# Kernel optimization log

Measured on AMD Instinct MI355X. Metric: run time of the kernel, lower is better.

The kernel has to match this reference:

```python
import jax, jax.numpy as jnp
import numpy as np

EPS = 0.1
B, D, H = 1048576, 2, 64


def _lagrangian(xs, W0, b0, W1, b1, W2, b2, W3, b3):
    # xs: [2] single sample -> scalar Lagrangian L(q, v)
    h = jnp.tanh(xs @ W0 + b0)
    h = jnp.tanh(h @ W1 + b1)
    h = jnp.tanh(h @ W2 + b2)
    return (h @ W3 + b3)[0]


def setup_inputs() -> dict:
    key = jax.random.key(0)
    ks = jax.random.split(key, 9)
    def lin(k, fan_in, fan_out):
        # mimic nn.Linear default init U(-1/sqrt(fan_in), 1/sqrt(fan_in))
        bound = 1.0 / np.sqrt(fan_in)
        kw, kb = jax.random.split(k)
        W = jax.random.uniform(kw, (fan_in, fan_out), jnp.float32, -bound, bound)
        b = jax.random.uniform(kb, (fan_out,), jnp.float32, -bound, bound)
        return W, b
    W0, b0 = lin(ks[1], D, H)
    W1, b1 = lin(ks[2], H, H)
    W2, b2 = lin(ks[3], H, H)
    W3, b3 = lin(ks[4], H, 1)
    x = jax.random.normal(ks[0], (B, D), jnp.float32)
    return {"t": 0, "x": x, "W0": W0, "b0": b0, "W1": W1, "b1": b1,
            "W2": W2, "b2": b2, "W3": W3, "b3": b3}


def reference(t, x, W0, b0, W1, b1, W2, b2, W3, b3):
    lag = lambda xs: _lagrangian(xs, W0, b0, W1, b1, W2, b2, W3, b3)
    grad_all = jax.vmap(jax.grad(lag))(x)          # [B, 2]
    H_full = jax.vmap(jax.hessian(lag))(x)          # [B, 2, 2]
    dL_dq = grad_all[:, 0:1]                        # [B, 1]
    d2L_dqv = H_full[:, 1, 0:1]                     # d2L/(dv dq)
    d2L_dv2 = H_full[:, 1, 1:2]                     # d2L/dv2
    v = x[:, 1:2]
    a = (dL_dq - d2L_dqv * v) / (d2L_dv2 + EPS)
    return jnp.concatenate([v, a], axis=1)          # [B, 2]
```

## Files before the change

### kernel.cpp

```cpp
#include <hip/hip_runtime.h>
#include <hip/hip_fp16.h>

typedef _Float16 half8 __attribute__((ext_vector_type(8)));
typedef float    f32x4 __attribute__((ext_vector_type(4)));
typedef float    f32x2 __attribute__((ext_vector_type(2)));

#define EPSL 0.1f
#define TWO_LOG2E 2.8853900817779268f
#define NT 4

#if __has_builtin(__builtin_amdgcn_exp2f)
#define EXP2(x) __builtin_amdgcn_exp2f(x)
#else
#define EXP2(x) __expf((x) * 0.6931471805599453f)
#endif

__device__ __forceinline__ f32x2 tanh2s(f32x2 y) {
    f32x2 e;
    e.x = EXP2(y.x);
    e.y = EXP2(y.y);
    const f32x2 ep = e + 1.0f;
    f32x2 r;
    r.x = __builtin_amdgcn_rcpf(ep.x);
    r.y = __builtin_amdgcn_rcpf(ep.y);
    return 1.0f - 2.0f * r;
}

__device__ __forceinline__ unsigned int pk2(float a, float b) {
    union { __fp16 __attribute__((ext_vector_type(2))) h; unsigned int u; } v;
    v.h = __builtin_amdgcn_cvt_pkrtz(a, b);
    return v.u;
}
__device__ __forceinline__ f32x2 unpk2v(unsigned int u) {
    union { unsigned int u; __half2 h; } v; v.u = u;
    const float2 f = __half22float2(v.h);
    return (f32x2){f.x, f.y};
}
__device__ __forceinline__ f32x2 lo2(f32x4 v) { return __builtin_shufflevector(v, v, 0, 1); }
__device__ __forceinline__ f32x2 hi2(f32x4 v) { return __builtin_shufflevector(v, v, 2, 3); }

union frag_u { unsigned int u[4]; half8 h; };

__global__ void pack_weights(const float* __restrict__ W1,
                             const float* __restrict__ W2,
                             _Float16* __restrict__ pk) {
    const int t = threadIdx.x;
    const int combo = blockIdx.x;
    const int mt  = combo & 3;
    const int kt  = (combo >> 2) & 1;
    const int mat = combo >> 3;
    const int q = t >> 4, r = t & 15;
    _Float16 v[8];
    #pragma unroll
    for (int j = 0; j < 8; ++j) {
        const int fk = (2 * kt + (j >> 2)) * 16 + 4 * q + (j & 3);
        float x;
        if (mat == 0)      x = W1[(kt * 32 + 8 * q + j) * 64 + mt * 16 + r];
        else if (mat == 1) x = W2[fk * 64 + mt * 16 + r];
        else if (mat == 2) x = W2[(mt * 16 + r) * 64 + fk];
        else {
            const int f0 = (mt & 1) * 32 + 8 * (r >> 2) + ((mt >> 1) & 1) * 4 + (r & 3);
            x = W1[f0 * 64 + fk];
        }
        v[j] = (_Float16)x;
    }
    *(half8*)(pk + combo * 512 + t * 8) = *(const half8*)v;
}

extern "C" __global__ void __launch_bounds__(256)
lnn_mfma(const float* __restrict__ x,
         const float* __restrict__ W0, const float* __restrict__ b0,
         const float* __restrict__ b1, const float* __restrict__ b2,
         const float* __restrict__ W3,
         const _Float16* __restrict__ pk,
         float* __restrict__ out)
{
    __shared__ float occ_pad[19456];
    if (blockIdx.x == 0xFFFFFFFFu) ((volatile float*)occ_pad)[threadIdx.x] = 1.0f;

    const int t = threadIdx.x & 63;
    const int q = t >> 4;
    const int r = t & 15;
    const long sbase = (long)blockIdx.x * (64 * NT) + (threadIdx.x >> 6) * (16 * NT);

    float x0v[NT], x1v[NT];
    #pragma unroll
    for (int u = 0; u < NT; ++u) {
        const float2 xv = *(const float2*)(x + 2 * (sbase + u * 16 + r));
        x0v[u] = xv.x; x1v[u] = xv.y;
    }

    auto ldpk = [&](int mat, int kt, int mt) -> half8 {
        return *(const half8*)(pk + ((mat * 2 + kt) * 4 + mt) * 512 + t * 8);
    };

    half8 ah0[NT][2], at0[NT][2];
    #pragma unroll
    for (int kt = 0; kt < 2; ++kt) {
        const int f = kt * 32 + q * 8;
        const float4 waA = *(const float4*)(W0 + f);
        const float4 waB = *(const float4*)(W0 + f + 4);
        const float4 wbA = *(const float4*)(W0 + 64 + f);
        const float4 wbB = *(const float4*)(W0 + 64 + f + 4);
        const float4 bbA = *(const float4*)(b0 + f);
        const float4 bbB = *(const float4*)(b0 + f + 4);
        const f32x2 wa2[4] = {{waA.x,waA.y},{waA.z,waA.w},{waB.x,waB.y},{waB.z,waB.w}};
        const f32x2 wb2[4] = {{wbA.x,wbA.y},{wbA.z,wbA.w},{wbB.x,wbB.y},{wbB.z,wbB.w}};
        const f32x2 bb2[4] = {{bbA.x,bbA.y},{bbA.z,bbA.w},{bbB.x,bbB.y},{bbB.z,bbB.w}};
        #pragma unroll
        for (int u = 0; u < NT; ++u) {
            union { unsigned int uu[4]; half8 h; } ph, pt;
            #pragma unroll
            for (int p = 0; p < 4; ++p) {
                const f32x2 z = x0v[u] * wa2[p] + x1v[u] * wb2[p] + bb2[p];
                const f32x2 h = tanh2s(z * TWO_LOG2E);
                const f32x2 A = 1.0f - h * h;
                const f32x2 tt = A * wb2[p];
                ph.uu[p] = pk2(h.x, h.y);
                pt.uu[p] = pk2(tt.x, tt.y);
            }
            ah0[u][kt] = ph.h; at0[u][kt] = pt.h;
        }
    }

    f32x4 acc[NT][4], tacc[NT][4];
    #pragma unroll
    for (int mt = 0; mt < 4; ++mt) {
        const f32x4 bv = *(const f32x4*)(b1 + mt * 16 + 4 * q);
        #pragma unroll
        for (int u = 0; u < NT; ++u) {
            acc[u][mt] = bv;
            tacc[u][mt] = (f32x4){0,0,0,0};
        }
    }
    #pragma unroll
    for (int kt = 0; kt < 2; ++kt)
        #pragma unroll
        for (int mt = 0; mt < 4; ++mt) {
            const half8 aw = ldpk(0, kt, mt);
            #pragma unroll
            for (int u = 0; u < NT; ++u) {
                acc[u][mt]  = __builtin_amdgcn_mfma_f32_16x16x32_f16(aw, ah0[u][kt], acc[u][mt], 0, 0, 0);
                tacc[u][mt] = __builtin_amdgcn_mfma_f32_16x16x32_f16(aw, at0[u][kt], tacc[u][mt], 0, 0, 0);
            }
        }

    frag_u bh1[NT][2], bt1[NT][2];
    #pragma unroll
    for (int u = 0; u < NT; ++u)
        #pragma unroll
        for (int mt = 0; mt < 4; ++mt) {
            const f32x2 zp[2] = {lo2(acc[u][mt]),  hi2(acc[u][mt])};
            const f32x2 tp[2] = {lo2(tacc[u][mt]), hi2(tacc[u][mt])};
            #pragma unroll
            for (int p = 0; p < 2; ++p) {
                const f32x2 h  = tanh2s(zp[p] * TWO_LOG2E);
                const f32x2 A  = 1.0f - h * h;
                const f32x2 th = A * tp[p];
                bh1[u][mt >> 1].u[2 * (mt & 1) + p] = pk2(h.x, h.y);
                bt1[u][mt >> 1].u[2 * (mt & 1) + p] = pk2(th.x, th.y);
            }
        }

    #pragma unroll
    for (int mt = 0; mt < 4; ++mt) {
        const f32x4 bv = *(const f32x4*)(b2 + mt * 16 + 4 * q);
        #pragma unroll
        for (int u = 0; u < NT; ++u) {
            acc[u][mt] = bv;
            tacc[u][mt] = (f32x4){0,0,0,0};
        }
    }
    #pragma unroll
    for (int kt = 0; kt < 2; ++kt)
        #pragma unroll
        for (int mt = 0; mt < 4; ++mt) {
            const half8 aw = ldpk(1, kt, mt);
            #pragma unroll
            for (int u = 0; u < NT; ++u) {
                acc[u][mt]  = __builtin_amdgcn_mfma_f32_16x16x32_f16(aw, bh1[u][kt].h, acc[u][mt], 0, 0, 0);
                tacc[u][mt] = __builtin_amdgcn_mfma_f32_16x16x32_f16(aw, bt1[u][kt].h, tacc[u][mt], 0, 0, 0);
            }
        }

    frag_u bh2[NT][2], bt2[NT][2];
    #pragma unroll
    for (int mt = 0; mt < 4; ++mt) {
        const float4 w3v = *(const float4*)(W3 + mt * 16 + 4 * q);
        const f32x2 w3p[2] = {{w3v.x, w3v.y}, {w3v.z, w3v.w}};
        #pragma unroll
        for (int u = 0; u < NT; ++u) {
            const f32x2 zp[2] = {lo2(acc[u][mt]),  hi2(acc[u][mt])};
            const f32x2 tp[2] = {lo2(tacc[u][mt]), hi2(tacc[u][mt])};
            #pragma unroll
            for (int p = 0; p < 2; ++p) {
                const f32x2 h  = tanh2s(zp[p] * TWO_LOG2E);
                const f32x2 A  = 1.0f - h * h;
                const f32x2 dz = A * w3p[p];
                const f32x2 t1 = h * tp[p];
                const f32x2 td = -2.0f * (dz * t1);
                bh2[u][mt >> 1].u[2 * (mt & 1) + p] = pk2(dz.x, dz.y);
                bt2[u][mt >> 1].u[2 * (mt & 1) + p] = pk2(td.x, td.y);
            }
        }
    }

    #pragma unroll
    for (int u = 0; u < NT; ++u)
        #pragma unroll
        for (int mt = 0; mt < 4; ++mt) { acc[u][mt] = (f32x4){0,0,0,0}; tacc[u][mt] = (f32x4){0,0,0,0}; }
    #pragma unroll
    for (int kt = 0; kt < 2; ++kt)
        #pragma unroll
        for (int mt = 0; mt < 4; ++mt) {
            const half8 aw = ldpk(2, kt, mt);
            #pragma unroll
            for (int u = 0; u < NT; ++u) {
                acc[u][mt]  = __builtin_amdgcn_mfma_f32_16x16x32_f16(aw, bh2[u][kt].h, acc[u][mt], 0, 0, 0);
                tacc[u][mt] = __builtin_amdgcn_mfma_f32_16x16x32_f16(aw, bt2[u][kt].h, tacc[u][mt], 0, 0, 0);
            }
        }

    frag_u bd[NT][2], btd[NT][2];
    #pragma unroll
    for (int u = 0; u < NT; ++u)
        #pragma unroll
        for (int mt = 0; mt < 4; ++mt) {
            const f32x2 gp[2] = {lo2(acc[u][mt]),  hi2(acc[u][mt])};
            const f32x2 tp[2] = {lo2(tacc[u][mt]), hi2(tacc[u][mt])};
            #pragma unroll
            for (int p = 0; p < 2; ++p) {
                const f32x2 h  = unpk2v(bh1[u][mt >> 1].u[2 * (mt & 1) + p]);
                const f32x2 th = unpk2v(bt1[u][mt >> 1].u[2 * (mt & 1) + p]);
                const f32x2 A  = 1.0f - h * h;
                const f32x2 d1 = gp[p] * A;
                const f32x2 u2 = (gp[p] * h) * th;
                const f32x2 td = tp[p] * A + (-2.0f) * u2;
                bd[u][mt >> 1].u[2 * (mt & 1) + p]  = pk2(d1.x, d1.y);
                btd[u][mt >> 1].u[2 * (mt & 1) + p] = pk2(td.x, td.y);
            }
        }

    #pragma unroll
    for (int u = 0; u < NT; ++u)
        #pragma unroll
        for (int mt = 0; mt < 4; ++mt) { acc[u][mt] = (f32x4){0,0,0,0}; tacc[u][mt] = (f32x4){0,0,0,0}; }
    #pragma unroll
    for (int kt = 0; kt < 2; ++kt)
        #pragma unroll
        for (int mt = 0; mt < 4; ++mt) {
            const half8 aw = ldpk(3, kt, mt);
            #pragma unroll
            for (int u = 0; u < NT; ++u) {
                acc[u][mt]  = __builtin_amdgcn_mfma_f32_16x16x32_f16(aw, bd[u][kt].h,  acc[u][mt], 0, 0, 0);
                tacc[u][mt] = __builtin_amdgcn_mfma_f32_16x16x32_f16(aw, btd[u][kt].h, tacc[u][mt], 0, 0, 0);
            }
        }

    f32x2 pg2[NT], ph02[NT], ph12[NT];
    #pragma unroll
    for (int u = 0; u < NT; ++u) { pg2[u] = (f32x2){0,0}; ph02[u] = (f32x2){0,0}; ph12[u] = (f32x2){0,0}; }
    #pragma unroll
    for (int mt = 0; mt < 4; ++mt) {
        const int kt = mt & 1;
        const int jb = ((mt >> 1) & 1) * 4;
        const int f  = kt * 32 + q * 8 + jb;
        const float4 waF = *(const float4*)(W0 + f);
        const float4 wbF = *(const float4*)(W0 + 64 + f);
        const f32x2 wa2[2] = {{waF.x, waF.y}, {waF.z, waF.w}};
        const f32x2 wb2[2] = {{wbF.x, wbF.y}, {wbF.z, wbF.w}};
        #pragma unroll
        for (int u = 0; u < NT; ++u) {
            union { half8 h; unsigned int uu[4]; } av; av.h = ah0[u][kt];
            const unsigned int hu[2] = {av.uu[jb >> 1], av.uu[(jb >> 1) + 1]};
            const f32x2 gp[2] = {lo2(acc[u][mt]),  hi2(acc[u][mt])};
            const f32x2 tp[2] = {lo2(tacc[u][mt]), hi2(tacc[u][mt])};
            #pragma unroll
            for (int p = 0; p < 2; ++p) {
                const f32x2 h   = unpk2v(hu[p]);
                const f32x2 A   = 1.0f - h * h;
                const f32x2 th0 = A * wb2[p];
                const f32x2 d0  = gp[p] * A;
                const f32x2 u2  = (gp[p] * h) * th0;
                const f32x2 td0 = tp[p] * A + (-2.0f) * u2;
                pg2[u]  += wa2[p] * d0;
                ph02[u] += wa2[p] * td0;
                ph12[u] += wb2[p] * td0;
            }
        }
    }
    #pragma unroll
    for (int u = 0; u < NT; ++u) {
        float pg  = pg2[u].x  + pg2[u].y;
        float ph0 = ph02[u].x + ph02[u].y;
        float ph1 = ph12[u].x + ph12[u].y;
        pg  += __shfl_xor(pg, 16);  pg  += __shfl_xor(pg, 32);
        ph0 += __shfl_xor(ph0, 16); ph0 += __shfl_xor(ph0, 32);
        ph1 += __shfl_xor(ph1, 16); ph1 += __shfl_xor(ph1, 32);
        if (q == 0) {
            const float num = fmaf(-ph0, x1v[u], pg);
            const float den = ph1 + EPSL;
            const float a = num * __builtin_amdgcn_rcpf(den);
            float2 o;
            o.x = x1v[u];
            o.y = a;
            *(float2*)(out + 2 * (sbase + u * 16 + r)) = o;
        }
    }
}

extern "C" void kernel_launch(void* const* d_in, const int* in_sizes, int n_in,
                              void* d_out, int out_size, void* d_ws, size_t ws_size,
                              hipStream_t stream) {
    const float* x  = (const float*)d_in[1];
    const float* W0 = (const float*)d_in[2];
    const float* b0 = (const float*)d_in[3];
    const float* W1 = (const float*)d_in[4];
    const float* b1 = (const float*)d_in[5];
    const float* W2 = (const float*)d_in[6];
    const float* b2 = (const float*)d_in[7];
    const float* W3 = (const float*)d_in[8];

    _Float16* pk = (_Float16*)d_ws;
    const int B = in_sizes[1] / 2;

    pack_weights<<<32, 64, 0, stream>>>(W1, W2, pk);
    lnn_mfma<<<B / (64 * NT), 256, 0, stream>>>(x, W0, b0, b1, b2, W3, pk, (float*)d_out);
}
```

Before: 215.0 us.

## Switch to persistent grid-stride waves with fewer tiles per wave

Turns the kernel into a persistent one: 768 blocks loop over 16*NT-sample tasks per wave, and the layer-0 weights and biases are hoisted into registers once per thread. NT drops from 4 to 2, which cuts per-wave accumulator register pressure, and the LDS occupancy pad shrinks to match the new occupancy target. The aim is better latency hiding and less launch/tail cost. The risk is less MFMA instruction-level parallelism per wave and a fixed grid size that may not match the CU count.

```diff
diff --git a/kernel.cpp b/kernel.cpp
--- a/kernel.cpp
+++ b/kernel.cpp
@@ -7,7 +7,7 @@
 
 #define EPSL 0.1f
 #define TWO_LOG2E 2.8853900817779268f
-#define NT 4
+#define NT 2
 
 #if __has_builtin(__builtin_amdgcn_exp2f)
 #define EXP2(x) __builtin_amdgcn_exp2f(x)
@@ -73,28 +73,23 @@
          const float* __restrict__ b1, const float* __restrict__ b2,
          const float* __restrict__ W3,
          const _Float16* __restrict__ pk,
-         float* __restrict__ out)
+         float* __restrict__ out,
+         int ntask)
 {
-    __shared__ float occ_pad[19456];
+    __shared__ float occ_pad[13312];
     if (blockIdx.x == 0xFFFFFFFFu) ((volatile float*)occ_pad)[threadIdx.x] = 1.0f;
 
     const int t = threadIdx.x & 63;
     const int q = t >> 4;
     const int r = t & 15;
-    const long sbase = (long)blockIdx.x * (64 * NT) + (threadIdx.x >> 6) * (16 * NT);
-
-    float x0v[NT], x1v[NT];
-    #pragma unroll
-    for (int u = 0; u < NT; ++u) {
-        const float2 xv = *(const float2*)(x + 2 * (sbase + u * 16 + r));
-        x0v[u] = xv.x; x1v[u] = xv.y;
-    }
+    const int wgid = blockIdx.x * 4 + (threadIdx.x >> 6);
+    const int nw   = gridDim.x * 4;
 
     auto ldpk = [&](int mat, int kt, int mt) -> half8 {
         return *(const half8*)(pk + ((mat * 2 + kt) * 4 + mt) * 512 + t * 8);
     };
 
-    half8 ah0[NT][2], at0[NT][2];
+    f32x2 wa2[2][4], wb2[2][4], bb2[2][4];
     #pragma unroll
     for (int kt = 0; kt < 2; ++kt) {
         const int f = kt * 32 + q * 8;
@@ -104,207 +99,220 @@
         const float4 wbB = *(const float4*)(W0 + 64 + f + 4);
         const float4 bbA = *(const float4*)(b0 + f);
         const float4 bbB = *(const float4*)(b0 + f + 4);
-        const f32x2 wa2[4] = {{waA.x,waA.y},{waA.z,waA.w},{waB.x,waB.y},{waB.z,waB.w}};
-        const f32x2 wb2[4] = {{wbA.x,wbA.y},{wbA.z,wbA.w},{wbB.x,wbB.y},{wbB.z,wbB.w}};
-        const f32x2 bb2[4] = {{bbA.x,bbA.y},{bbA.z,bbA.w},{bbB.x,bbB.y},{bbB.z,bbB.w}};
+        wa2[kt][0] = (f32x2){waA.x, waA.y}; wa2[kt][1] = (f32x2){waA.z, waA.w};
+        wa2[kt][2] = (f32x2){waB.x, waB.y}; wa2[kt][3] = (f32x2){waB.z, waB.w};
+        wb2[kt][0] = (f32x2){wbA.x, wbA.y}; wb2[kt][1] = (f32x2){wbA.z, wbA.w};
+        wb2[kt][2] = (f32x2){wbB.x, wbB.y}; wb2[kt][3] = (f32x2){wbB.z, wbB.w};
+        bb2[kt][0] = (f32x2){bbA.x, bbA.y}; bb2[kt][1] = (f32x2){bbA.z, bbA.w};
+        bb2[kt][2] = (f32x2){bbB.x, bbB.y}; bb2[kt][3] = (f32x2){bbB.z, bbB.w};
+    }
+
+    for (int task = wgid; task < ntask; task += nw) {
+        const long sbase = (long)task * (16 * NT);
+
+        float x0v[NT], x1v[NT];
         #pragma unroll
         for (int u = 0; u < NT; ++u) {
-            union { unsigned int uu[4]; half8 h; } ph, pt;
-            #pragma unroll
-            for (int p = 0; p < 4; ++p) {
-                const f32x2 z = x0v[u] * wa2[p] + x1v[u] * wb2[p] + bb2[p];
-                const f32x2 h = tanh2s(z * TWO_LOG2E);
-                const f32x2 A = 1.0f - h * h;
-                const f32x2 tt = A * wb2[p];
-                ph.uu[p] = pk2(h.x, h.y);
-                pt.uu[p] = pk2(tt.x, tt.y);
-            }
-            ah0[u][kt] = ph.h; at0[u][kt] = pt.h;
-        }
-    }
-
-    f32x4 acc[NT][4], tacc[NT][4];
-    #pragma unroll
-    for (int mt = 0; mt < 4; ++mt) {
-        const f32x4 bv = *(const f32x4*)(b1 + mt * 16 + 4 * q);
+            const float2 xv = *(const float2*)(x + 2 * (sbase + u * 16 + r));
+            x0v[u] = xv.x; x1v[u] = xv.y;
+        }
+
+        half8 ah0[NT][2], at0[NT][2];
+        #pragma unroll
+        for (int kt = 0; kt < 2; ++kt)
+            #pragma unroll
+            for (int u = 0; u < NT; ++u) {
+                union { unsigned int uu[4]; half8 h; } ph, pt;
+                #pragma unroll
+                for (int p = 0; p < 4; ++p) {
+                    const f32x2 z = x0v[u] * wa2[kt][p] + x1v[u] * wb2[kt][p] + bb2[kt][p];
+                    const f32x2 h = tanh2s(z * TWO_LOG2E);
+                    const f32x2 A = 1.0f - h * h;
+                    const f32x2 tt = A * wb2[kt][p];
+                    ph.uu[p] = pk2(h.x, h.y);
+                    pt.uu[p] = pk2(tt.x, tt.y);
+                }
+                ah0[u][kt] = ph.h; at0[u][kt] = pt.h;
+            }
+
+        f32x4 acc[NT][4], tacc[NT][4];
+        #pragma unroll
+        for (int mt = 0; mt < 4; ++mt) {
+            const f32x4 bv = *(const f32x4*)(b1 + mt * 16 + 4 * q);
+            #pragma unroll
+            for (int u = 0; u < NT; ++u) {
+                acc[u][mt] = bv;
+                tacc[u][mt] = (f32x4){0,0,0,0};
+            }
+        }
+        #pragma unroll
+        for (int kt = 0; kt < 2; ++kt)
+            #pragma unroll
+            for (int mt = 0; mt < 4; ++mt) {
+                const half8 aw = ldpk(0, kt, mt);
+                #pragma unroll
+                for (int u = 0; u < NT; ++u) {
+                    acc[u][mt]  = __builtin_amdgcn_mfma_f32_16x16x32_f16(aw, ah0[u][kt], acc[u][mt], 0, 0, 0);
+                    tacc[u][mt] = __builtin_amdgcn_mfma_f32_16x16x32_f16(aw, at0[u][kt], tacc[u][mt], 0, 0, 0);
+                }
+            }
+
+        frag_u bh1[NT][2], bt1[NT][2];
+        #pragma unroll
+        for (int u = 0; u < NT; ++u)
+            #pragma unroll
+            for (int mt = 0; mt < 4; ++mt) {
+                const f32x2 zp[2] = {lo2(acc[u][mt]),  hi2(acc[u][mt])};
+                const f32x2 tp[2] = {lo2(tacc[u][mt]), hi2(tacc[u][mt])};
+                #pragma unroll
+                for (int p = 0; p < 2; ++p) {
+                    const f32x2 h  = tanh2s(zp[p] * TWO_LOG2E);
+                    const f32x2 A  = 1.0f - h * h;
+                    const f32x2 th = A * tp[p];
+                    bh1[u][mt >> 1].u[2 * (mt & 1) + p] = pk2(h.x, h.y);
+                    bt1[u][mt >> 1].u[2 * (mt & 1) + p] = pk2(th.x, th.y);
+                }
+            }
+
+        #pragma unroll
+        for (int mt = 0; mt < 4; ++mt) {
+            const f32x4 bv = *(const f32x4*)(b2 + mt * 16 + 4 * q);
+            #pragma unroll
+            for (int u = 0; u < NT; ++u) {
+                acc[u][mt] = bv;
+                tacc[u][mt] = (f32x4){0,0,0,0};
+            }
+        }
+        #pragma unroll
+        for (int kt = 0; kt < 2; ++kt)
+            #pragma unroll
+            for (int mt = 0; mt < 4; ++mt) {
+                const half8 aw = ldpk(1, kt, mt);
+                #pragma unroll
+                for (int u = 0; u < NT; ++u) {
+                    acc[u][mt]  = __builtin_amdgcn_mfma_f32_16x16x32_f16(aw, bh1[u][kt].h, acc[u][mt], 0, 0, 0);
+                    tacc[u][mt] = __builtin_amdgcn_mfma_f32_16x16x32_f16(aw, bt1[u][kt].h, tacc[u][mt], 0, 0, 0);
+                }
+            }
+
+        frag_u bh2[NT][2], bt2[NT][2];
+        #pragma unroll
+        for (int mt = 0; mt < 4; ++mt) {
+            const float4 w3v = *(const float4*)(W3 + mt * 16 + 4 * q);
+            const f32x2 w3p[2] = {{w3v.x, w3v.y}, {w3v.z, w3v.w}};
+            #pragma unroll
+            for (int u = 0; u < NT; ++u) {
+                const f32x2 zp[2] = {lo2(acc[u][mt]),  hi2(acc[u][mt])};
+                const f32x2 tp[2] = {lo2(tacc[u][mt]), hi2(tacc[u][mt])};
+                #pragma unroll
+                for (int p = 0; p < 2; ++p) {
+                    const f32x2 h  = tanh2s(zp[p] * TWO_LOG2E);
+                    const f32x2 A  = 1.0f - h * h;
+                    const f32x2 dz = A * w3p[p];
+                    const f32x2 t1 = h * tp[p];
+                    const f32x2 td = -2.0f * (dz * t1);
+                    bh2[u][mt >> 1].u[2 * (mt & 1) + p] = pk2(dz.x, dz.y);
+                    bt2[u][mt >> 1].u[2 * (mt & 1) + p] = pk2(td.x, td.y);
+                }
+            }
+        }
+
+        #pragma unroll
+        for (int u = 0; u < NT; ++u)
+            #pragma unroll
+            for (int mt = 0; mt < 4; ++mt) { acc[u][mt] = (f32x4){0,0,0,0}; tacc[u][mt] = (f32x4){0,0,0,0}; }
+        #pragma unroll
+        for (int kt = 0; kt < 2; ++kt)
+            #pragma unroll
+            for (int mt = 0; mt < 4; ++mt) {
+                const half8 aw = ldpk(2, kt, mt);
+                #pragma unroll
+                for (int u = 0; u < NT; ++u) {
+                    acc[u][mt]  = __builtin_amdgcn_mfma_f32_16x16x32_f16(aw, bh2[u][kt].h, acc[u][mt], 0, 0, 0);
+                    tacc[u][mt] = __builtin_amdgcn_mfma_f32_16x16x32_f16(aw, bt2[u][kt].h, tacc[u][mt], 0, 0, 0);
+                }
+            }
+
+        frag_u bd[NT][2], btd[NT][2];
+        #pragma unroll
+        for (int u = 0; u < NT; ++u)
+            #pragma unroll
+            for (int mt = 0; mt < 4; ++mt) {
+                const f32x2 gp[2] = {lo2(acc[u][mt]),  hi2(acc[u][mt])};
+                const f32x2 tp[2] = {lo2(tacc[u][mt]), hi2(tacc[u][mt])};
+                #pragma unroll
+                for (int p = 0; p < 2; ++p) {
+                    const f32x2 h  = unpk2v(bh1[u][mt >> 1].u[2 * (mt & 1) + p]);
+                    const f32x2 th = unpk2v(bt1[u][mt >> 1].u[2 * (mt & 1) + p]);
+                    const f32x2 A  = 1.0f - h * h;
+                    const f32x2 d1 = gp[p] * A;
+                    const f32x2 u2 = (gp[p] * h) * th;
+                    const f32x2 td = tp[p] * A + (-2.0f) * u2;
+                    bd[u][mt >> 1].u[2 * (mt & 1) + p]  = pk2(d1.x, d1.y);
+                    btd[u][mt >> 1].u[2 * (mt & 1) + p] = pk2(td.x, td.y);
+                }
+            }
+
+        #pragma unroll
+        for (int u = 0; u < NT; ++u)
+            #pragma unroll
+            for (int mt = 0; mt < 4; ++mt) { acc[u][mt] = (f32x4){0,0,0,0}; tacc[u][mt] = (f32x4){0,0,0,0}; }
+        #pragma unroll
+        for (int kt = 0; kt < 2; ++kt)
+            #pragma unroll
+            for (int mt = 0; mt < 4; ++mt) {
+                const half8 aw = ldpk(3, kt, mt);
+                #pragma unroll
+                for (int u = 0; u < NT; ++u) {
+                    acc[u][mt]  = __builtin_amdgcn_mfma_f32_16x16x32_f16(aw, bd[u][kt].h,  acc[u][mt], 0, 0, 0);
+                    tacc[u][mt] = __builtin_amdgcn_mfma_f32_16x16x32_f16(aw, btd[u][kt].h, tacc[u][mt], 0, 0, 0);
+                }
+            }
+
+        f32x2 pg2[NT], ph02[NT], ph12[NT];
+        #pragma unroll
+        for (int u = 0; u < NT; ++u) { pg2[u] = (f32x2){0,0}; ph02[u] = (f32x2){0,0}; ph12[u] = (f32x2){0,0}; }
+        #pragma unroll
+        for (int mt = 0; mt < 4; ++mt) {
+            const int kt = mt & 1;
+            const int j2 = ((mt >> 1) & 1) * 2;
+            #pragma unroll
+            for (int u = 0; u < NT; ++u) {
+                union { half8 h; unsigned int uu[4]; } av; av.h = ah0[u][kt];
+                const unsigned int hu[2] = {av.uu[j2], av.uu[j2 + 1]};
+                const f32x2 gp[2] = {lo2(acc[u][mt]),  hi2(acc[u][mt])};
+                const f32x2 tp[2] = {lo2(tacc[u][mt]), hi2(tacc[u][mt])};
+                #pragma unroll
+                for (int p = 0; p < 2; ++p) {
+                    const f32x2 h   = unpk2v(hu[p]);
+                    const f32x2 A   = 1.0f - h * h;
+                    const f32x2 th0 = A * wb2[kt][j2 + p];
+                    const f32x2 d0  = gp[p] * A;
+                    const f32x2 u2  = (gp[p] * h) * th0;
+                    const f32x2 td0 = tp[p] * A + (-2.0f) * u2;
+                    pg2[u]  += wa2[kt][j2 + p] * d0;
+                    ph02[u] += wa2[kt][j2 + p] * td0;
+                    ph12[u] += wb2[kt][j2 + p] * td0;
+                }
+            }
+        }
         #pragma unroll
         for (int u = 0; u < NT; ++u) {
-            acc[u][mt] = bv;
-            tacc[u][mt] = (f32x4){0,0,0,0};
-        }
-    }
-    #pragma unroll
-    for (int kt = 0; kt < 2; ++kt)
-        #pragma unroll
-        for (int mt = 0; mt < 4; ++mt) {
-            const half8 aw = ldpk(0, kt, mt);
-            #pragma unroll
-            for (int u = 0; u < NT; ++u) {
-                acc[u][mt]  = __builtin_amdgcn_mfma_f32_16x16x32_f16(aw, ah0[u][kt], acc[u][mt], 0, 0, 0);
-                tacc[u][mt] = __builtin_amdgcn_mfma_f32_16x16x32_f16(aw, at0[u][kt], tacc[u][mt], 0, 0, 0);
-            }
-        }
-
-    frag_u bh1[NT][2], bt1[NT][2];
-    #pragma unroll
-    for (int u = 0; u < NT; ++u)
-        #pragma unroll
-        for (int mt = 0; mt < 4; ++mt) {
-            const f32x2 zp[2] = {lo2(acc[u][mt]),  hi2(acc[u][mt])};
-            const f32x2 tp[2] = {lo2(tacc[u][mt]), hi2(tacc[u][mt])};
-            #pragma unroll
-            for (int p = 0; p < 2; ++p) {
-                const f32x2 h  = tanh2s(zp[p] * TWO_LOG2E);
-                const f32x2 A  = 1.0f - h * h;
-                const f32x2 th = A * tp[p];
-                bh1[u][mt >> 1].u[2 * (mt & 1) + p] = pk2(h.x, h.y);
-                bt1[u][mt >> 1].u[2 * (mt & 1) + p] = pk2(th.x, th.y);
-            }
-        }
-
-    #pragma unroll
-    for (int mt = 0; mt < 4; ++mt) {
-        const f32x4 bv = *(const f32x4*)(b2 + mt * 16 + 4 * q);
-        #pragma unroll
-        for (int u = 0; u < NT; ++u) {
-            acc[u][mt] = bv;
-            tacc[u][mt] = (f32x4){0,0,0,0};
-        }
-    }
-    #pragma unroll
-    for (int kt = 0; kt < 2; ++kt)
-        #pragma unroll
-        for (int mt = 0; mt < 4; ++mt) {
-            const half8 aw = ldpk(1, kt, mt);
-            #pragma unroll
-            for (int u = 0; u < NT; ++u) {
-                acc[u][mt]  = __builtin_amdgcn_mfma_f32_16x16x32_f16(aw, bh1[u][kt].h, acc[u][mt], 0, 0, 0);
-                tacc[u][mt] = __builtin_amdgcn_mfma_f32_16x16x32_f16(aw, bt1[u][kt].h, tacc[u][mt], 0, 0, 0);
-            }
-        }
-
-    frag_u bh2[NT][2], bt2[NT][2];
-    #pragma unroll
-    for (int mt = 0; mt < 4; ++mt) {
-        const float4 w3v = *(const float4*)(W3 + mt * 16 + 4 * q);
-        const f32x2 w3p[2] = {{w3v.x, w3v.y}, {w3v.z, w3v.w}};
-        #pragma unroll
-        for (int u = 0; u < NT; ++u) {
-            const f32x2 zp[2] = {lo2(acc[u][mt]),  hi2(acc[u][mt])};
-            const f32x2 tp[2] = {lo2(tacc[u][mt]), hi2(tacc[u][mt])};
-            #pragma unroll
-            for (int p = 0; p < 2; ++p) {
-                const f32x2 h  = tanh2s(zp[p] * TWO_LOG2E);
-                const f32x2 A  = 1.0f - h * h;
-                const f32x2 dz = A * w3p[p];
-                const f32x2 t1 = h * tp[p];
-                const f32x2 td = -2.0f * (dz * t1);
-                bh2[u][mt >> 1].u[2 * (mt & 1) + p] = pk2(dz.x, dz.y);
-                bt2[u][mt >> 1].u[2 * (mt & 1) + p] = pk2(td.x, td.y);
-            }
-        }
-    }
-
-    #pragma unroll
-    for (int u = 0; u < NT; ++u)
-        #pragma unroll
-        for (int mt = 0; mt < 4; ++mt) { acc[u][mt] = (f32x4){0,0,0,0}; tacc[u][mt] = (f32x4){0,0,0,0}; }
-    #pragma unroll
-    for (int kt = 0; kt < 2; ++kt)
-        #pragma unroll
-        for (int mt = 0; mt < 4; ++mt) {
-            const half8 aw = ldpk(2, kt, mt);
-            #pragma unroll
-            for (int u = 0; u < NT; ++u) {
-                acc[u][mt]  = __builtin_amdgcn_mfma_f32_16x16x32_f16(aw, bh2[u][kt].h, acc[u][mt], 0, 0, 0);
-                tacc[u][mt] = __builtin_amdgcn_mfma_f32_16x16x32_f16(aw, bt2[u][kt].h, tacc[u][mt], 0, 0, 0);
-            }
-        }
-
-    frag_u bd[NT][2], btd[NT][2];
-    #pragma unroll
-    for (int u = 0; u < NT; ++u)
-        #pragma unroll
-        for (int mt = 0; mt < 4; ++mt) {
-            const f32x2 gp[2] = {lo2(acc[u][mt]),  hi2(acc[u][mt])};
-            const f32x2 tp[2] = {lo2(tacc[u][mt]), hi2(tacc[u][mt])};
-            #pragma unroll
-            for (int p = 0; p < 2; ++p) {
-                const f32x2 h  = unpk2v(bh1[u][mt >> 1].u[2 * (mt & 1) + p]);
-                const f32x2 th = unpk2v(bt1[u][mt >> 1].u[2 * (mt & 1) + p]);
-                const f32x2 A  = 1.0f - h * h;
-                const f32x2 d1 = gp[p] * A;
-                const f32x2 u2 = (gp[p] * h) * th;
-                const f32x2 td = tp[p] * A + (-2.0f) * u2;
-                bd[u][mt >> 1].u[2 * (mt & 1) + p]  = pk2(d1.x, d1.y);
-                btd[u][mt >> 1].u[2 * (mt & 1) + p] = pk2(td.x, td.y);
-            }
-        }
-
-    #pragma unroll
-    for (int u = 0; u < NT; ++u)
-        #pragma unroll
-        for (int mt = 0; mt < 4; ++mt) { acc[u][mt] = (f32x4){0,0,0,0}; tacc[u][mt] = (f32x4){0,0,0,0}; }
-    #pragma unroll
-    for (int kt = 0; kt < 2; ++kt)
-        #pragma unroll
-        for (int mt = 0; mt < 4; ++mt) {
-            const half8 aw = ldpk(3, kt, mt);
-            #pragma unroll
-            for (int u = 0; u < NT; ++u) {
-                acc[u][mt]  = __builtin_amdgcn_mfma_f32_16x16x32_f16(aw, bd[u][kt].h,  acc[u][mt], 0, 0, 0);
-                tacc[u][mt] = __builtin_amdgcn_mfma_f32_16x16x32_f16(aw, btd[u][kt].h, tacc[u][mt], 0, 0, 0);
-            }
-        }
-
-    f32x2 pg2[NT], ph02[NT], ph12[NT];
-    #pragma unroll
-    for (int u = 0; u < NT; ++u) { pg2[u] = (f32x2){0,0}; ph02[u] = (f32x2){0,0}; ph12[u] = (f32x2){0,0}; }
-    #pragma unroll
-    for (int mt = 0; mt < 4; ++mt) {
-        const int kt = mt & 1;
-        const int jb = ((mt >> 1) & 1) * 4;
-        const int f  = kt * 32 + q * 8 + jb;
-        const float4 waF = *(const float4*)(W0 + f);
-        const float4 wbF = *(const float4*)(W0 + 64 + f);
-        const f32x2 wa2[2] = {{waF.x, waF.y}, {waF.z, waF.w}};
-        const f32x2 wb2[2] = {{wbF.x, wbF.y}, {wbF.z, wbF.w}};
-        #pragma unroll
-        for (int u = 0; u < NT; ++u) {
-            union { half8 h; unsigned int uu[4]; } av; av.h = ah0[u][kt];
-            const unsigned int hu[2] = {av.uu[jb >> 1], av.uu[(jb >> 1) + 1]};
-            const f32x2 gp[2] = {lo2(acc[u][mt]),  hi2(acc[u][mt])};
-            const f32x2 tp[2] = {lo2(tacc[u][mt]), hi2(tacc[u][mt])};
-            #pragma unroll
-            for (int p = 0; p < 2; ++p) {
-                const f32x2 h   = unpk2v(hu[p]);
-                const f32x2 A   = 1.0f - h * h;
-                const f32x2 th0 = A * wb2[p];
-                const f32x2 d0  = gp[p] * A;
-                const f32x2 u2  = (gp[p] * h) * th0;
-                const f32x2 td0 = tp[p] * A + (-2.0f) * u2;
-                pg2[u]  += wa2[p] * d0;
-                ph02[u] += wa2[p] * td0;
-                ph12[u] += wb2[p] * td0;
-            }
-        }
-    }
-    #pragma unroll
-    for (int u = 0; u < NT; ++u) {
-        float pg  = pg2[u].x  + pg2[u].y;
-        float ph0 = ph02[u].x + ph02[u].y;
-        float ph1 = ph12[u].x + ph12[u].y;
-        pg  += __shfl_xor(pg, 16);  pg  += __shfl_xor(pg, 32);
-        ph0 += __shfl_xor(ph0, 16); ph0 += __shfl_xor(ph0, 32);
-        ph1 += __shfl_xor(ph1, 16); ph1 += __shfl_xor(ph1, 32);
-        if (q == 0) {
-            const float num = fmaf(-ph0, x1v[u], pg);
-            const float den = ph1 + EPSL;
-            const float a = num * __builtin_amdgcn_rcpf(den);
-            float2 o;
-            o.x = x1v[u];
-            o.y = a;
-            *(float2*)(out + 2 * (sbase + u * 16 + r)) = o;
+            float pg  = pg2[u].x  + pg2[u].y;
+            float ph0 = ph02[u].x + ph02[u].y;
+            float ph1 = ph12[u].x + ph12[u].y;
+            pg  += __shfl_xor(pg, 16);  pg  += __shfl_xor(pg, 32);
+            ph0 += __shfl_xor(ph0, 16); ph0 += __shfl_xor(ph0, 32);
+            ph1 += __shfl_xor(ph1, 16); ph1 += __shfl_xor(ph1, 32);
+            if (q == 0) {
+                const float num = fmaf(-ph0, x1v[u], pg);
+                const float den = ph1 + EPSL;
+                const float a = num * __builtin_amdgcn_rcpf(den);
+                float2 o;
+                o.x = x1v[u];
+                o.y = a;
+                *(float2*)(out + 2 * (sbase + u * 16 + r)) = o;
+            }
         }
     }
 }
@@ -323,7 +331,8 @@
 
     _Float16* pk = (_Float16*)d_ws;
     const int B = in_sizes[1] / 2;
+    const int ntask = B / (16 * NT);
 
     pack_weights<<<32, 64, 0, stream>>>(W1, W2, pk);
-    lnn_mfma<<<B / (64 * NT), 256, 0, stream>>>(x, W0, b0, b1, b2, W3, pk, (float*)d_out);
-}
+    lnn_mfma<<<768, 256, 0, stream>>>(x, W0, b0, b1, b2, W3, pk, (float*)d_out, ntask);
+}
```

Measured after the change: 217.8 us. No clear change (+1.3%).
